# Performance work log

Hardware: AMD Instinct MI355X
Metric: run time of the kernel (lower is better)

Reference implementation:

```python
import jax, jax.numpy as jnp
import numpy as np
import math

N = 30000
E = 600000
IN_DIM = 256
HID = 64
EMB = 64
HEADS = 4
EPS = 1e-5


def _glorot(key, shape):
    fan_in, fan_out = shape[0], shape[1]
    lim = math.sqrt(6.0 / (fan_in + fan_out))
    return jax.random.uniform(key, shape, jnp.float32, -lim, lim)


def setup_inputs() -> dict:
    key = jax.random.key(0)
    ks = jax.random.split(key, 24)
    inp = {
        "x": jax.random.normal(ks[0], (N, IN_DIM), jnp.float32),
        "edge_index": jax.random.randint(ks[1], (2, E), 0, N, jnp.int64),
    }
    # layer 1: in=IN_DIM, out per head=HID, heads=HEADS -> width HID*HEADS
    w1 = HID * HEADS
    inp.update({
        "w1q": _glorot(ks[2], (IN_DIM, w1)), "b1q": jnp.zeros((w1,), jnp.float32),
        "w1k": _glorot(ks[3], (IN_DIM, w1)), "b1k": jnp.zeros((w1,), jnp.float32),
        "w1v": _glorot(ks[4], (IN_DIM, w1)), "b1v": jnp.zeros((w1,), jnp.float32),
        "w1s": _glorot(ks[5], (IN_DIM, w1)), "b1s": jnp.zeros((w1,), jnp.float32),
        "g1": jnp.ones((w1,), jnp.float32), "be1": jnp.zeros((w1,), jnp.float32),
    })
    # layer 2: in=HID*HEADS, out per head=EMB -> width EMB*HEADS
    w2 = EMB * HEADS
    inp.update({
        "w2q": _glorot(ks[6], (w1, w2)), "b2q": jnp.zeros((w2,), jnp.float32),
        "w2k": _glorot(ks[7], (w1, w2)), "b2k": jnp.zeros((w2,), jnp.float32),
        "w2v": _glorot(ks[8], (w1, w2)), "b2v": jnp.zeros((w2,), jnp.float32),
        "w2s": _glorot(ks[9], (w1, w2)), "b2s": jnp.zeros((w2,), jnp.float32),
        "g2": jnp.ones((w2,), jnp.float32), "be2": jnp.zeros((w2,), jnp.float32),
    })
    return inp


def transformer_conv(x, edge_index, wq, bq, wk, bk, wv, bv, ws, bs, heads, out_ch):
    n = x.shape[0]
    q = (x @ wq + bq).reshape(n, heads, out_ch)
    k = (x @ wk + bk).reshape(n, heads, out_ch)
    v = (x @ wv + bv).reshape(n, heads, out_ch)
    src, dst = edge_index[0], edge_index[1]
    # per-edge gather: [E, H, C]
    qi, kj, vj = q[dst], k[src], v[src]
    alpha = jnp.sum(qi * kj, axis=-1) / math.sqrt(out_ch)  # [E, H]
    # segment softmax over incoming edges of each target node
    amax = jax.lax.stop_gradient(jax.ops.segment_max(alpha, dst, num_segments=n))
    ex = jnp.exp(alpha - amax[dst])
    denom = jax.ops.segment_sum(ex, dst, num_segments=n)
    alpha = ex / denom[dst]
    # scatter-add weighted values back to targets
    out = jax.ops.segment_sum(vj * alpha[..., None], dst, num_segments=n)
    out = out.reshape(n, heads * out_ch)
    return out + x @ ws + bs  # root/skip connection


def batch_norm(x, gamma, beta):
    mean = jnp.mean(x, axis=0)
    var = jnp.mean(jnp.square(x - mean), axis=0)  # biased, training-mode BN
    return (x - mean) * jax.lax.rsqrt(var + EPS) * gamma + beta


def leaky_relu(x):
    return jnp.where(x >= 0, x, 0.1 * x)


def reference(x, edge_index, w1q, b1q, w1k, b1k, w1v, b1v, w1s, b1s, g1, be1,
              w2q, b2q, w2k, b2k, w2v, b2v, w2s, b2s, g2, be2):
    h = transformer_conv(x, edge_index, w1q, b1q, w1k, b1k, w1v, b1v, w1s, b1s, HEADS, HID)
    h = leaky_relu(batch_norm(h, g1, be1))
    h = transformer_conv(h, edge_index, w2q, b2q, w2k, b2k, w2v, b2v, w2s, b2s, HEADS, EMB)
    h = leaky_relu(batch_norm(h, g2, be2))
    return h
```

## Files before the change

kernel.cpp:

```cpp
#include <hip/hip_runtime.h>
#include <math.h>

#define NODES 30000
#define EDGES 600000
#define QKVS_W 1024
#define OUT_W 256
#define BN_EPS 1e-5f

typedef __attribute__((ext_vector_type(8))) __bf16 bf16x8;
typedef __attribute__((ext_vector_type(4))) float f32x4;

__device__ __forceinline__ unsigned short f2bf(float f) {
    union { float f; unsigned int u; } v; v.f = f;
    unsigned int r = v.u + 0x7FFFu + ((v.u >> 16) & 1u);
    return (unsigned short)(r >> 16);
}
__device__ __forceinline__ float bf2f(unsigned short u) {
    union { unsigned int u; float f; } v; v.u = ((unsigned int)u) << 16;
    return v.f;
}

typedef const __attribute__((address_space(1))) void* gas_p;
typedef __attribute__((address_space(3))) void* las_p;
__device__ __forceinline__ void gload_lds16(const void* g, void* l) {
    __builtin_amdgcn_global_load_lds((gas_p)g, (las_p)l, 16, 0, 0);
}


__global__ __launch_bounds__(256) void k_count(const int* __restrict__ ei, int* __restrict__ deg) {
    int e = blockIdx.x * 256 + threadIdx.x;
    if (e < EDGES) atomicAdd(&deg[ei[EDGES + e]], 1);
}

__global__ __launch_bounds__(256) void k_blocksum(const int* __restrict__ deg, int* __restrict__ bsum) {
    __shared__ int sh[256];
    int i = blockIdx.x * 256 + threadIdx.x;
    sh[threadIdx.x] = (i < NODES) ? deg[i] : 0;
    __syncthreads();
    for (int off = 128; off > 0; off >>= 1) {
        if (threadIdx.x < off) sh[threadIdx.x] += sh[threadIdx.x + off];
        __syncthreads();
    }
    if (threadIdx.x == 0) bsum[blockIdx.x] = sh[0];
}

__global__ __launch_bounds__(128) void k_scanb(const int* __restrict__ bsum, int* __restrict__ bbase, int nb) {
    __shared__ int sh[128];
    int t = threadIdx.x;
    int v = (t < nb) ? bsum[t] : 0;
    sh[t] = v;
    __syncthreads();
    for (int off = 1; off < 128; off <<= 1) {
        int add = (t >= off) ? sh[t - off] : 0;
        __syncthreads();
        sh[t] += add;
        __syncthreads();
    }
    if (t < nb) bbase[t] = sh[t] - v;
}

__global__ __launch_bounds__(256) void k_localscan(const int* __restrict__ deg, const int* __restrict__ bbase,
                                                   int* __restrict__ rowptr, int* __restrict__ cursor) {
    __shared__ int sh[256];
    int i = blockIdx.x * 256 + threadIdx.x;
    int v = (i < NODES) ? deg[i] : 0;
    sh[threadIdx.x] = v;
    __syncthreads();
    for (int off = 1; off < 256; off <<= 1) {
        int add = (threadIdx.x >= off) ? sh[threadIdx.x - off] : 0;
        __syncthreads();
        sh[threadIdx.x] += add;
        __syncthreads();
    }
    if (i < NODES) {
        int p = bbase[blockIdx.x] + sh[threadIdx.x] - v;
        rowptr[i] = p;
        cursor[i] = p;
    }
}

__global__ __launch_bounds__(256) void k_fill(const int* __restrict__ ei, int* __restrict__ cursor,
                                              int* __restrict__ csr_src) {
    int e = blockIdx.x * 256 + threadIdx.x;
    if (e < EDGES) {
        int s = ei[e];
        int d = ei[EDGES + e];
        int slot = atomicAdd(&cursor[d], 1);
        csr_src[slot] = s;
    }
}


__global__ __launch_bounds__(256) void k_castA(const float* __restrict__ in, unsigned short* __restrict__ out, int n8) {
    int i = blockIdx.x * 256 + threadIdx.x;
    if (i >= n8) return;
    const float4* p = (const float4*)(in + (size_t)i * 8);
    float4 v0 = p[0], v1 = p[1];
    ushort4 o0, o1;
    o0.x = f2bf(v0.x); o0.y = f2bf(v0.y); o0.z = f2bf(v0.z); o0.w = f2bf(v0.w);
    o1.x = f2bf(v1.x); o1.y = f2bf(v1.y); o1.z = f2bf(v1.z); o1.w = f2bf(v1.w);
    ushort4* q = (ushort4*)(out + (size_t)i * 8);
    q[0] = o0; q[1] = o1;
}

__global__ __launch_bounds__(256) void k_castW2(
    const float* __restrict__ Wa0, const float* __restrict__ Wa1,
    const float* __restrict__ Wa2, const float* __restrict__ Wa3,
    const float* __restrict__ Ba0, const float* __restrict__ Ba1,
    const float* __restrict__ Ba2, const float* __restrict__ Ba3,
    const float* __restrict__ Wb0, const float* __restrict__ Wb1,
    const float* __restrict__ Wb2, const float* __restrict__ Wb3,
    const float* __restrict__ Bb0, const float* __restrict__ Bb1,
    const float* __restrict__ Bb2, const float* __restrict__ Bb3,
    unsigned short* __restrict__ Wt1, float* __restrict__ bf1,
    unsigned short* __restrict__ Wt2, float* __restrict__ bf2)
{
    int nn0 = blockIdx.x;
    int layer = nn0 >> 10;
    int n = nn0 & 1023;
    int k = threadIdx.x;
    int wsel = n >> 8, nc = n & 255;
    const float* W; const float* Bv;
    if (layer == 0) {
        W  = (wsel == 0) ? Wa0 : (wsel == 1) ? Wa1 : (wsel == 2) ? Wa2 : Wa3;
        Bv = (wsel == 0) ? Ba0 : (wsel == 1) ? Ba1 : (wsel == 2) ? Ba2 : Ba3;
    } else {
        W  = (wsel == 0) ? Wb0 : (wsel == 1) ? Wb1 : (wsel == 2) ? Wb2 : Wb3;
        Bv = (wsel == 0) ? Bb0 : (wsel == 1) ? Bb1 : (wsel == 2) ? Bb2 : Bb3;
    }
    unsigned short* Wt = (layer == 0) ? Wt1 : Wt2;
    float* bfused = (layer == 0) ? bf1 : bf2;
    Wt[(size_t)n * 256 + k] = f2bf(W[(size_t)k * 256 + nc]);
    if (k == 0) bfused[n] = Bv[nc];
}


#define CS 136

__global__ __launch_bounds__(256) void k_gemm_bf16(
    const unsigned short* __restrict__ A,
    const unsigned short* __restrict__ Wt,
    const float* __restrict__ bias,
    unsigned short* __restrict__ C, int M)
{
    __shared__ unsigned short sbuf[128 * CS];
    unsigned short* As = sbuf;
    unsigned short* Bs = sbuf + 8192;
    int tid = threadIdx.x;
    int lane = tid & 63;
    int wave = tid >> 6;
    int wm = wave & 1, wn = wave >> 1;
    int row0 = blockIdx.x * 128;
    int n0 = blockIdx.y * 128;

    f32x4 acc[4][4] = {};

    for (int k0 = 0; k0 < 256; k0 += 64) {
        #pragma unroll
        for (int w = 0; w < 4; w++) {
            int c = w * 256 + tid;
            int row = c >> 3;
            int cole = (c & 7) * 8;
            int ar = row0 + row; if (ar >= M) ar = M - 1;
            gload_lds16(&A[(size_t)ar * 256 + k0 + cole], &As[w * 2048 + tid * 8]);
            gload_lds16(&Wt[(size_t)(n0 + row) * 256 + k0 + cole], &Bs[w * 2048 + tid * 8]);
        }
        __syncthreads();
        int rsel = lane & 15;
        int kq = (lane >> 4) * 8;
        #pragma unroll
        for (int kh = 0; kh < 2; kh++) {
            bf16x8 af[4], bf[4];
            #pragma unroll
            for (int t = 0; t < 4; t++) {
                af[t] = *reinterpret_cast<const bf16x8*>(&As[(wm * 64 + t * 16 + rsel) * 64 + kh * 32 + kq]);
                bf[t] = *reinterpret_cast<const bf16x8*>(&Bs[(wn * 64 + t * 16 + rsel) * 64 + kh * 32 + kq]);
            }
            #pragma unroll
            for (int mt = 0; mt < 4; mt++)
                #pragma unroll
                for (int nt = 0; nt < 4; nt++)
                    acc[mt][nt] = __builtin_amdgcn_mfma_f32_16x16x32_bf16(af[mt], bf[nt], acc[mt][nt], 0, 0, 0);
        }
        __syncthreads();
    }

    int crow = (lane >> 4) * 4;
    int ccol = lane & 15;
    #pragma unroll
    for (int mt = 0; mt < 4; mt++) {
        int lrow = wm * 64 + mt * 16 + crow;
        #pragma unroll
        for (int nt = 0; nt < 4; nt++) {
            int lcol = wn * 64 + nt * 16 + ccol;
            float bv = bias[n0 + lcol];
            #pragma unroll
            for (int r = 0; r < 4; r++)
                sbuf[(lrow + r) * CS + lcol] = f2bf(acc[mt][nt][r] + bv);
        }
    }
    __syncthreads();
    int chunk = tid & 15;
    int rbase = tid >> 4;
    #pragma unroll
    for (int g = 0; g < 8; g++) {
        int row_l = g * 16 + rbase;
        int gr = row0 + row_l;
        if (gr < M) {
            uint4 val = *(const uint4*)&sbuf[row_l * CS + chunk * 8];
            *(uint4*)&C[(size_t)gr * QKVS_W + n0 + chunk * 8] = val;
        }
    }
}


__global__ __launch_bounds__(256) void k_attn_bf16(const unsigned short* __restrict__ qkvs,
                                                   const int* __restrict__ rowptr,
                                                   const int* __restrict__ deg,
                                                   const int* __restrict__ csr_src,
                                                   float* __restrict__ out)
{
    int wave = threadIdx.x >> 6;
    int lane = threadIdx.x & 63;
    int node = blockIdx.x * 4 + wave;
    if (node >= NODES) return;

    const unsigned short* qrow = qkvs + (size_t)node * QKVS_W;
    float q0, q1, q2, q3;
    {
        ushort4 qv = *(const ushort4*)&qrow[lane * 4];
        q0 = bf2f(qv.x); q1 = bf2f(qv.y); q2 = bf2f(qv.z); q3 = bf2f(qv.w);
    }

    float m = -INFINITY, L = 0.f;
    float a0 = 0.f, a1 = 0.f, a2 = 0.f, a3 = 0.f;

    int start = rowptr[node];
    int cnt = deg[node];

    ushort4 kA, vA, kB, vB;
    if (cnt > 0) {
        const unsigned short* p = qkvs + (size_t)csr_src[start] * QKVS_W;
        kA = *(const ushort4*)&p[256 + lane * 4];
        vA = *(const ushort4*)&p[512 + lane * 4];
    }
    if (cnt > 1) {
        const unsigned short* p = qkvs + (size_t)csr_src[start + 1] * QKVS_W;
        kB = *(const ushort4*)&p[256 + lane * 4];
        vB = *(const ushort4*)&p[512 + lane * 4];
    }
    int e = 0;
    for (; e + 1 < cnt; e += 2) {
        ushort4 nkA, nvA, nkB, nvB;
        if (e + 2 < cnt) {
            const unsigned short* p = qkvs + (size_t)csr_src[start + e + 2] * QKVS_W;
            nkA = *(const ushort4*)&p[256 + lane * 4];
            nvA = *(const ushort4*)&p[512 + lane * 4];
        }
        if (e + 3 < cnt) {
            const unsigned short* p = qkvs + (size_t)csr_src[start + e + 3] * QKVS_W;
            nkB = *(const ushort4*)&p[256 + lane * 4];
            nvB = *(const ushort4*)&p[512 + lane * 4];
        }
        float d1 = q0 * bf2f(kA.x) + q1 * bf2f(kA.y) + q2 * bf2f(kA.z) + q3 * bf2f(kA.w);
        float d2 = q0 * bf2f(kB.x) + q1 * bf2f(kB.y) + q2 * bf2f(kB.z) + q3 * bf2f(kB.w);
        d1 += __shfl_xor(d1, 1, 64);  d2 += __shfl_xor(d2, 1, 64);
        d1 += __shfl_xor(d1, 2, 64);  d2 += __shfl_xor(d2, 2, 64);
        d1 += __shfl_xor(d1, 4, 64);  d2 += __shfl_xor(d2, 4, 64);
        d1 += __shfl_xor(d1, 8, 64);  d2 += __shfl_xor(d2, 8, 64);
        float al1 = d1 * 0.125f;
        float al2 = d2 * 0.125f;
        float nm = fmaxf(m, fmaxf(al1, al2));
        float sc = __expf(m - nm);
        float p1 = __expf(al1 - nm);
        float p2 = __expf(al2 - nm);
        L  = L * sc + p1 + p2;
        a0 = a0 * sc + p1 * bf2f(vA.x) + p2 * bf2f(vB.x);
        a1 = a1 * sc + p1 * bf2f(vA.y) + p2 * bf2f(vB.y);
        a2 = a2 * sc + p1 * bf2f(vA.z) + p2 * bf2f(vB.z);
        a3 = a3 * sc + p1 * bf2f(vA.w) + p2 * bf2f(vB.w);
        m = nm;
        kA = nkA; vA = nvA; kB = nkB; vB = nvB;
    }
    if (e < cnt) {
        float d1 = q0 * bf2f(kA.x) + q1 * bf2f(kA.y) + q2 * bf2f(kA.z) + q3 * bf2f(kA.w);
        d1 += __shfl_xor(d1, 1, 64);
        d1 += __shfl_xor(d1, 2, 64);
        d1 += __shfl_xor(d1, 4, 64);
        d1 += __shfl_xor(d1, 8, 64);
        float al1 = d1 * 0.125f;
        float nm = fmaxf(m, al1);
        float sc = __expf(m - nm);
        float p1 = __expf(al1 - nm);
        L  = L * sc + p1;
        a0 = a0 * sc + p1 * bf2f(vA.x);
        a1 = a1 * sc + p1 * bf2f(vA.y);
        a2 = a2 * sc + p1 * bf2f(vA.z);
        a3 = a3 * sc + p1 * bf2f(vA.w);
    }

    float inv = (L > 0.f) ? 1.f / L : 0.f;
    ushort4 sv = *(const ushort4*)&qrow[768 + lane * 4];
    float4 o;
    o.x = a0 * inv + bf2f(sv.x);
    o.y = a1 * inv + bf2f(sv.y);
    o.z = a2 * inv + bf2f(sv.z);
    o.w = a3 * inv + bf2f(sv.w);
    *(float4*)&out[(size_t)node * OUT_W + lane * 4] = o;
}


__global__ __launch_bounds__(256) void k_bnstats(const float* __restrict__ h,
                                                 float* __restrict__ sum, float* __restrict__ sumsq) {
    int col = threadIdx.x;
    int r0 = blockIdx.x * 64;
    int r1 = min(r0 + 64, NODES);
    float s = 0.f, s2 = 0.f;
    for (int r = r0; r < r1; r++) {
        float v = h[(size_t)r * OUT_W + col];
        s += v; s2 += v * v;
    }
    atomicAdd(&sum[col], s);
    atomicAdd(&sumsq[col], s2);
}

__device__ __forceinline__ float4 bn_scale4(const float* sum, const float* sumsq,
                                            const float* g, const float* be,
                                            int col, float4* shift) {
    float4 s  = *(const float4*)&sum[col];
    float4 s2 = *(const float4*)&sumsq[col];
    float4 gv = *(const float4*)&g[col];
    float4 bv = *(const float4*)&be[col];
    const float invN = 1.0f / NODES;
    float4 sc, sh;
    float mean, var;
    mean = s.x * invN; var = fmaxf(s2.x * invN - mean * mean, 0.f);
    sc.x = gv.x * rsqrtf(var + BN_EPS); sh.x = bv.x - mean * sc.x;
    mean = s.y * invN; var = fmaxf(s2.y * invN - mean * mean, 0.f);
    sc.y = gv.y * rsqrtf(var + BN_EPS); sh.y = bv.y - mean * sc.y;
    mean = s.z * invN; var = fmaxf(s2.z * invN - mean * mean, 0.f);
    sc.z = gv.z * rsqrtf(var + BN_EPS); sh.z = bv.z - mean * sc.z;
    mean = s.w * invN; var = fmaxf(s2.w * invN - mean * mean, 0.f);
    sc.w = gv.w * rsqrtf(var + BN_EPS); sh.w = bv.w - mean * sc.w;
    *shift = sh;
    return sc;
}

__global__ __launch_bounds__(256) void k_bnapply_bf16(const float* __restrict__ h,
                                                      const float* __restrict__ sum,
                                                      const float* __restrict__ sumsq,
                                                      const float* __restrict__ g,
                                                      const float* __restrict__ be,
                                                      unsigned short* __restrict__ out) {
    int idx = blockIdx.x * 256 + threadIdx.x;
    int base = idx * 4;
    int col = base & (OUT_W - 1);
    float4 sh;
    float4 sc = bn_scale4(sum, sumsq, g, be, col, &sh);
    float4 v = *(const float4*)&h[base];
    float4 o;
    o.x = v.x * sc.x + sh.x; o.x = (o.x >= 0.f) ? o.x : 0.1f * o.x;
    o.y = v.y * sc.y + sh.y; o.y = (o.y >= 0.f) ? o.y : 0.1f * o.y;
    o.z = v.z * sc.z + sh.z; o.z = (o.z >= 0.f) ? o.z : 0.1f * o.z;
    o.w = v.w * sc.w + sh.w; o.w = (o.w >= 0.f) ? o.w : 0.1f * o.w;
    ushort4 u; u.x = f2bf(o.x); u.y = f2bf(o.y); u.z = f2bf(o.z); u.w = f2bf(o.w);
    *(ushort4*)&out[base] = u;
}

__global__ __launch_bounds__(256) void k_bnapply(const float* __restrict__ h,
                                                 const float* __restrict__ sum,
                                                 const float* __restrict__ sumsq,
                                                 const float* __restrict__ g,
                                                 const float* __restrict__ be,
                                                 float* __restrict__ out) {
    int idx = blockIdx.x * 256 + threadIdx.x;
    int base = idx * 4;
    int col = base & (OUT_W - 1);
    float4 sh;
    float4 sc = bn_scale4(sum, sumsq, g, be, col, &sh);
    float4 v = *(const float4*)&h[base];
    float4 o;
    o.x = v.x * sc.x + sh.x; o.x = (o.x >= 0.f) ? o.x : 0.1f * o.x;
    o.y = v.y * sc.y + sh.y; o.y = (o.y >= 0.f) ? o.y : 0.1f * o.y;
    o.z = v.z * sc.z + sh.z; o.z = (o.z >= 0.f) ? o.z : 0.1f * o.z;
    o.w = v.w * sc.w + sh.w; o.w = (o.w >= 0.f) ? o.w : 0.1f * o.w;
    *(float4*)&out[base] = o;
}


extern "C" void kernel_launch(void* const* d_in, const int* in_sizes, int n_in,
                              void* d_out, int out_size, void* d_ws, size_t ws_size,
                              hipStream_t stream) {
    const float* x  = (const float*)d_in[0];
    const int*   ei = (const int*)d_in[1];
    const float* w1[4] = {(const float*)d_in[2], (const float*)d_in[4], (const float*)d_in[6], (const float*)d_in[8]};
    const float* b1[4] = {(const float*)d_in[3], (const float*)d_in[5], (const float*)d_in[7], (const float*)d_in[9]};
    const float* g1  = (const float*)d_in[10];
    const float* be1 = (const float*)d_in[11];
    const float* w2[4] = {(const float*)d_in[12], (const float*)d_in[14], (const float*)d_in[16], (const float*)d_in[18]};
    const float* b2[4] = {(const float*)d_in[13], (const float*)d_in[15], (const float*)d_in[17], (const float*)d_in[19]};
    const float* g2  = (const float*)d_in[20];
    const float* be2 = (const float*)d_in[21];

    char* ws = (char*)d_ws;
    unsigned short* qkvsb  = (unsigned short*)(ws);
    float*          h1     = (float*)(ws + 61440000);
    unsigned short* abuf   = (unsigned short*)(ws + 92160000);
    unsigned short* wt1    = (unsigned short*)(ws + 107520000);
    unsigned short* wt2    = (unsigned short*)(ws + 108044288);
    float*          b1f    = (float*)(ws + 108568576);
    float*          b2f    = (float*)(ws + 108572672);
    int*            deg    = (int*)  (ws + 108576768);
    int*            rowptr = (int*)  (ws + 108696768);
    int*            cursor = (int*)  (ws + 108816768);
    int*            csr    = (int*)  (ws + 108936768);
    int*            bsum   = (int*)  (ws + 111336768);
    int*            bbase  = (int*)  (ws + 111337280);
    float*          sum1   = (float*)(ws + 111337792);
    float*          sq1    = (float*)(ws + 111338816);
    float*          sum2   = (float*)(ws + 111339840);
    float*          sq2    = (float*)(ws + 111340864);

    hipMemsetAsync(deg, 0, NODES * sizeof(int), stream);
    hipMemsetAsync(sum1, 0, 4096, stream);

    const int EB = (EDGES + 255) / 256;
    const int NB = (NODES + 255) / 256;

    k_castA<<<(NODES * 256 / 8 + 255) / 256, 256, 0, stream>>>(x, abuf, NODES * 256 / 8);
    k_castW2<<<2048, 256, 0, stream>>>(w1[0], w1[1], w1[2], w1[3], b1[0], b1[1], b1[2], b1[3],
                                       w2[0], w2[1], w2[2], w2[3], b2[0], b2[1], b2[2], b2[3],
                                       wt1, b1f, wt2, b2f);

    k_count    <<<EB, 256, 0, stream>>>(ei, deg);
    k_blocksum <<<NB, 256, 0, stream>>>(deg, bsum);
    k_scanb    <<<1, 128, 0, stream>>>(bsum, bbase, NB);
    k_localscan<<<NB, 256, 0, stream>>>(deg, bbase, rowptr, cursor);
    k_fill     <<<EB, 256, 0, stream>>>(ei, cursor, csr);

    dim3 ggrid((NODES + 127) / 128, 8);
    const int ANB = NODES / 4;
    const int APB = (NODES * OUT_W / 4) / 256;
    const int SNB = (NODES + 63) / 64;

    k_gemm_bf16  <<<ggrid, 256, 0, stream>>>(abuf, wt1, b1f, qkvsb, NODES);
    k_attn_bf16  <<<ANB, 256, 0, stream>>>(qkvsb, rowptr, deg, csr, h1);
    k_bnstats    <<<SNB, 256, 0, stream>>>(h1, sum1, sq1);
    k_bnapply_bf16<<<APB, 256, 0, stream>>>(h1, sum1, sq1, g1, be1, abuf);

    k_gemm_bf16  <<<ggrid, 256, 0, stream>>>(abuf, wt2, b2f, qkvsb, NODES);
    k_attn_bf16  <<<ANB, 256, 0, stream>>>(qkvsb, rowptr, deg, csr, h1);
    k_bnstats    <<<SNB, 256, 0, stream>>>(h1, sum2, sq2);
    k_bnapply    <<<APB, 256, 0, stream>>>(h1, sum2, sq2, g2, be2, (float*)d_out);
}
```

Baseline: 519.6 us.

## Split attention wave into two half-waves processing alternate edges with lazy rescale

The per-node attention kernel now splits each 64-lane wave into two 32-lane halves. Each half handles alternate incoming edges, loading 8 bf16 values per lane with 16-byte loads, and a deeper rolling prefetch keeps the index and K/V gathers further ahead. The online softmax rescales only when some lane's logit exceeds the running max by more than 8, which saves most exp and multiply work on the accumulators. The two halves' partial max, sum and accumulators are merged with cross-half shuffles at the end. This cuts shuffle-reduction depth and instruction count per edge, at the cost of wasted lanes on odd-degree tails and more registers.

```diff
diff --git a/kernel.cpp b/kernel.cpp
--- a/kernel.cpp
+++ b/kernel.cpp
@@ -17,6 +17,14 @@
 }
 __device__ __forceinline__ float bf2f(unsigned short u) {
     union { unsigned int u; float f; } v; v.u = ((unsigned int)u) << 16;
+    return v.f;
+}
+__device__ __forceinline__ float bflo(unsigned int u) {
+    union { unsigned int u; float f; } v; v.u = u << 16;
+    return v.f;
+}
+__device__ __forceinline__ float bfhi(unsigned int u) {
+    union { unsigned int u; float f; } v; v.u = u & 0xffff0000u;
     return v.f;
 }
 
@@ -224,89 +232,122 @@
     int lane = threadIdx.x & 63;
     int node = blockIdx.x * 4 + wave;
     if (node >= NODES) return;
+    int half = lane >> 5;
+    int lh = lane & 31;
 
     const unsigned short* qrow = qkvs + (size_t)node * QKVS_W;
-    float q0, q1, q2, q3;
+    float qf0, qf1, qf2, qf3, qf4, qf5, qf6, qf7;
     {
-        ushort4 qv = *(const ushort4*)&qrow[lane * 4];
-        q0 = bf2f(qv.x); q1 = bf2f(qv.y); q2 = bf2f(qv.z); q3 = bf2f(qv.w);
-    }
-
-    float m = -INFINITY, L = 0.f;
-    float a0 = 0.f, a1 = 0.f, a2 = 0.f, a3 = 0.f;
+        uint4 qv = *(const uint4*)&qrow[lh * 8];
+        qf0 = bflo(qv.x); qf1 = bfhi(qv.x);
+        qf2 = bflo(qv.y); qf3 = bfhi(qv.y);
+        qf4 = bflo(qv.z); qf5 = bfhi(qv.z);
+        qf6 = bflo(qv.w); qf7 = bfhi(qv.w);
+    }
 
     int start = rowptr[node];
     int cnt = deg[node];
-
-    ushort4 kA, vA, kB, vB;
+    int npairs = (cnt + 1) >> 1;
+
+    float m = -INFINITY, L = 0.f;
+    float acc[8] = {0.f, 0.f, 0.f, 0.f, 0.f, 0.f, 0.f, 0.f};
+
     if (cnt > 0) {
-        const unsigned short* p = qkvs + (size_t)csr_src[start] * QKVS_W;
-        kA = *(const ushort4*)&p[256 + lane * 4];
-        vA = *(const ushort4*)&p[512 + lane * 4];
-    }
-    if (cnt > 1) {
-        const unsigned short* p = qkvs + (size_t)csr_src[start + 1] * QKVS_W;
-        kB = *(const ushort4*)&p[256 + lane * 4];
-        vB = *(const ushort4*)&p[512 + lane * 4];
-    }
-    int e = 0;
-    for (; e + 1 < cnt; e += 2) {
-        ushort4 nkA, nvA, nkB, nvB;
-        if (e + 2 < cnt) {
-            const unsigned short* p = qkvs + (size_t)csr_src[start + e + 2] * QKVS_W;
-            nkA = *(const ushort4*)&p[256 + lane * 4];
-            nvA = *(const ushort4*)&p[512 + lane * 4];
-        }
-        if (e + 3 < cnt) {
-            const unsigned short* p = qkvs + (size_t)csr_src[start + e + 3] * QKVS_W;
-            nkB = *(const ushort4*)&p[256 + lane * 4];
-            nvB = *(const ushort4*)&p[512 + lane * 4];
-        }
-        float d1 = q0 * bf2f(kA.x) + q1 * bf2f(kA.y) + q2 * bf2f(kA.z) + q3 * bf2f(kA.w);
-        float d2 = q0 * bf2f(kB.x) + q1 * bf2f(kB.y) + q2 * bf2f(kB.z) + q3 * bf2f(kB.w);
-        d1 += __shfl_xor(d1, 1, 64);  d2 += __shfl_xor(d2, 1, 64);
-        d1 += __shfl_xor(d1, 2, 64);  d2 += __shfl_xor(d2, 2, 64);
-        d1 += __shfl_xor(d1, 4, 64);  d2 += __shfl_xor(d2, 4, 64);
-        d1 += __shfl_xor(d1, 8, 64);  d2 += __shfl_xor(d2, 8, 64);
-        float al1 = d1 * 0.125f;
-        float al2 = d2 * 0.125f;
-        float nm = fmaxf(m, fmaxf(al1, al2));
-        float sc = __expf(m - nm);
-        float p1 = __expf(al1 - nm);
-        float p2 = __expf(al2 - nm);
-        L  = L * sc + p1 + p2;
-        a0 = a0 * sc + p1 * bf2f(vA.x) + p2 * bf2f(vB.x);
-        a1 = a1 * sc + p1 * bf2f(vA.y) + p2 * bf2f(vB.y);
-        a2 = a2 * sc + p1 * bf2f(vA.z) + p2 * bf2f(vB.z);
-        a3 = a3 * sc + p1 * bf2f(vA.w) + p2 * bf2f(vB.w);
-        m = nm;
-        kA = nkA; vA = nvA; kB = nkB; vB = nvB;
-    }
-    if (e < cnt) {
-        float d1 = q0 * bf2f(kA.x) + q1 * bf2f(kA.y) + q2 * bf2f(kA.z) + q3 * bf2f(kA.w);
-        d1 += __shfl_xor(d1, 1, 64);
-        d1 += __shfl_xor(d1, 2, 64);
-        d1 += __shfl_xor(d1, 4, 64);
-        d1 += __shfl_xor(d1, 8, 64);
-        float al1 = d1 * 0.125f;
-        float nm = fmaxf(m, al1);
-        float sc = __expf(m - nm);
-        float p1 = __expf(al1 - nm);
-        L  = L * sc + p1;
-        a0 = a0 * sc + p1 * bf2f(vA.x);
-        a1 = a1 * sc + p1 * bf2f(vA.y);
-        a2 = a2 * sc + p1 * bf2f(vA.z);
-        a3 = a3 * sc + p1 * bf2f(vA.w);
-    }
-
-    float inv = (L > 0.f) ? 1.f / L : 0.f;
-    ushort4 sv = *(const ushort4*)&qrow[768 + lane * 4];
+        int clast = cnt - 1;
+        int e0 = 0 * 2 + half; if (e0 > clast) e0 = clast;
+        int e1 = 1 * 2 + half; if (e1 > clast) e1 = clast;
+        int e2 = 2 * 2 + half; if (e2 > clast) e2 = clast;
+        int e3 = 3 * 2 + half; if (e3 > clast) e3 = clast;
+        int ix0 = csr_src[start + e0];
+        int ix1 = csr_src[start + e1];
+        int ix2 = csr_src[start + e2];
+        int ix3 = csr_src[start + e3];
+        uint4 k0v, v0v, k1v, v1v;
+        {
+            const unsigned short* p = qkvs + (size_t)ix0 * QKVS_W + lh * 8;
+            k0v = *(const uint4*)(p + 256);
+            v0v = *(const uint4*)(p + 512);
+        }
+        {
+            const unsigned short* p = qkvs + (size_t)ix1 * QKVS_W + lh * 8;
+            k1v = *(const uint4*)(p + 256);
+            v1v = *(const uint4*)(p + 512);
+        }
+        for (int i = 0; i < npairs; i++) {
+            int en = (i + 4) * 2 + half; if (en > clast) en = clast;
+            int ixn = csr_src[start + en];
+            uint4 knv, vnv;
+            {
+                const unsigned short* p = qkvs + (size_t)ix2 * QKVS_W + lh * 8;
+                knv = *(const uint4*)(p + 256);
+                vnv = *(const uint4*)(p + 512);
+            }
+            int e = 2 * i + half;
+            bool valid = e < cnt;
+            float d;
+            d = qf0 * bflo(k0v.x);
+            d = fmaf(qf1, bfhi(k0v.x), d);
+            d = fmaf(qf2, bflo(k0v.y), d);
+            d = fmaf(qf3, bfhi(k0v.y), d);
+            d = fmaf(qf4, bflo(k0v.z), d);
+            d = fmaf(qf5, bfhi(k0v.z), d);
+            d = fmaf(qf6, bflo(k0v.w), d);
+            d = fmaf(qf7, bfhi(k0v.w), d);
+            d += __shfl_xor(d, 1, 64);
+            d += __shfl_xor(d, 2, 64);
+            d += __shfl_xor(d, 4, 64);
+            float al = d * 0.125f;
+            if (valid) {
+                if (__any(al > m + 8.f)) {
+                    float nm = fmaxf(m, al);
+                    float sc = __expf(m - nm);
+                    L *= sc;
+                    #pragma unroll
+                    for (int j = 0; j < 8; j++) acc[j] *= sc;
+                    m = nm;
+                }
+                float p = __expf(al - m);
+                L += p;
+                acc[0] = fmaf(p, bflo(v0v.x), acc[0]);
+                acc[1] = fmaf(p, bfhi(v0v.x), acc[1]);
+                acc[2] = fmaf(p, bflo(v0v.y), acc[2]);
+                acc[3] = fmaf(p, bfhi(v0v.y), acc[3]);
+                acc[4] = fmaf(p, bflo(v0v.z), acc[4]);
+                acc[5] = fmaf(p, bfhi(v0v.z), acc[5]);
+                acc[6] = fmaf(p, bflo(v0v.w), acc[6]);
+                acc[7] = fmaf(p, bfhi(v0v.w), acc[7]);
+            }
+            k0v = k1v; v0v = v1v; k1v = knv; v1v = vnv;
+            ix2 = ix3; ix3 = ixn;
+        }
+    }
+
+    float mo = __shfl_xor(m, 32, 64);
+    float Lo = __shfl_xor(L, 32, 64);
+    float nm = fmaxf(m, mo);
+    float scs = (L  > 0.f) ? __expf(m  - nm) : 0.f;
+    float sco = (Lo > 0.f) ? __expf(mo - nm) : 0.f;
+    float Lt = fmaf(L, scs, Lo * sco);
+    float inv = (Lt > 0.f) ? 1.f / Lt : 0.f;
+    float t0 = fmaf(acc[0], scs, __shfl_xor(acc[0], 32, 64) * sco);
+    float t1 = fmaf(acc[1], scs, __shfl_xor(acc[1], 32, 64) * sco);
+    float t2 = fmaf(acc[2], scs, __shfl_xor(acc[2], 32, 64) * sco);
+    float t3 = fmaf(acc[3], scs, __shfl_xor(acc[3], 32, 64) * sco);
+    float t4 = fmaf(acc[4], scs, __shfl_xor(acc[4], 32, 64) * sco);
+    float t5 = fmaf(acc[5], scs, __shfl_xor(acc[5], 32, 64) * sco);
+    float t6 = fmaf(acc[6], scs, __shfl_xor(acc[6], 32, 64) * sco);
+    float t7 = fmaf(acc[7], scs, __shfl_xor(acc[7], 32, 64) * sco);
+    float w0 = half ? t4 : t0;
+    float w1 = half ? t5 : t1;
+    float w2 = half ? t6 : t2;
+    float w3 = half ? t7 : t3;
+    ushort4 sv = *(const ushort4*)&qrow[768 + lh * 8 + half * 4];
     float4 o;
-    o.x = a0 * inv + bf2f(sv.x);
-    o.y = a1 * inv + bf2f(sv.y);
-    o.z = a2 * inv + bf2f(sv.z);
-    o.w = a3 * inv + bf2f(sv.w);
-    *(float4*)&out[(size_t)node * OUT_W + lane * 4] = o;
+    o.x = fmaf(w0, inv, bf2f(sv.x));
+    o.y = fmaf(w1, inv, bf2f(sv.y));
+    o.z = fmaf(w2, inv, bf2f(sv.z));
+    o.w = fmaf(w3, inv, bf2f(sv.w));
+    *(float4*)&out[(size_t)node * OUT_W + lh * 8 + half * 4] = o;
 }
 
 
```

Measured after the change: 511.1 us. No clear change (-1.6%).
